# Performance work log

Hardware: AMD Instinct MI355X
Metric: run time of the kernel (lower is better)

## Reference

```python
import jax, jax.numpy as jnp
import numpy as np

ORDER = 3
N_LANES = 5  # lane ids 1..5 (0 = background)
EPS_DEN = 1e-5
RIDGE = 1e-6  # tiny jitter so the 4x4 normal-equation solve is well-posed (matches lstsq on full-rank data)


def setup_inputs() -> dict:
    key = jax.random.key(0)
    k1, k2 = jax.random.split(key)
    hnet_params = jax.random.normal(k1, (8, 6), dtype=jnp.float32)
    instance_label = jax.random.randint(k2, (8, 256, 512), 0, N_LANES + 1).astype(jnp.int64)
    return {"hnet_params": hnet_params, "instance_label": instance_label}


def reference(hnet_params, instance_label):
    B, Hh, Ww = instance_label.shape
    N = Hh * Ww
    p = hnet_params
    z = jnp.zeros((B,), p.dtype)
    o = jnp.ones((B,), p.dtype)
    # H = [[p0,p1,p2],[0,p3,p4],[0,p5,1]]
    Hm = jnp.stack([
        jnp.stack([p[:, 0], p[:, 1], p[:, 2]], -1),
        jnp.stack([z, p[:, 3], p[:, 4]], -1),
        jnp.stack([z, p[:, 5], o], -1),
    ], axis=1)  # [B,3,3]

    yy, xx = jnp.meshgrid(jnp.arange(Hh), jnp.arange(Ww), indexing='ij')
    P = jnp.stack([xx.reshape(-1), yy.reshape(-1), jnp.ones((N,), jnp.int32)]).astype(jnp.float32)  # [3,N]
    Pp = jnp.einsum('bij,jn->bin', Hm, P)  # [B,3,N]
    den = Pp[:, 2]
    den = jnp.where(jnp.abs(den) < EPS_DEN, jnp.full_like(den, EPS_DEN), den)
    xp = Pp[:, 0] / den  # [B,N]
    yp = Pp[:, 1] / den  # [B,N]

    exps = jnp.arange(ORDER, -1, -1)  # powers order..0
    Y = yp[..., None] ** exps  # [B,N,k]

    lane_ids = jnp.arange(1, N_LANES + 1)
    m = (instance_label.reshape(B, 1, N) == lane_ids[None, :, None]).astype(jnp.float32)  # [B,L,N]
    cnt = m.sum(-1)  # [B,L]
    cnt_safe = jnp.maximum(cnt, 1.0)

    # weighted normal equations per (batch, lane): (Y^T M Y) w = Y^T M x'
    A = jnp.einsum('bln,bni,bnj->blij', m, Y, Y)
    rhs = jnp.einsum('bln,bni,bn->bli', m, Y, xp)
    k = ORDER + 1
    A = A + RIDGE * jnp.eye(k, dtype=A.dtype)
    w = jnp.linalg.solve(A, rhs[..., None])[..., 0]  # [B,L,k]

    x_pred = jnp.einsum('bni,bli->bln', Y, w)  # [B,L,N]
    mse = (m * (xp[:, None, :] - x_pred) ** 2).sum(-1) / cnt_safe
    mad = (m * jnp.abs(den)[:, None, :]).sum(-1) / cnt_safe
    lane_loss = mse * mad  # [B,L]

    valid = (cnt >= ORDER + 1).astype(jnp.float32)
    nv = valid.sum()
    loss = jnp.where(nv > 0, (valid * lane_loss).sum() / jnp.maximum(nv, 1.0), 0.0)
    return loss
```

## Files before the change

### kernel.cpp

```cpp
#include <hip/hip_runtime.h>

#define BB 8
#define HH 256
#define WW 512
#define NLANES 5
#define KORD 4
#define RIDGE_D 1e-6
#define EPS_DEN_F 1e-5f

__global__ void row_hist_kernel(const int* __restrict__ labels,
                                int* __restrict__ stats) {
    const int row  = blockIdx.x;
    const int lane = threadIdx.x;
    const int* rp = labels + (size_t)row * WW;

    int c[NLANES], sx[NLANES], sxx[NLANES];
#pragma unroll
    for (int l = 0; l < NLANES; ++l) { c[l] = 0; sx[l] = 0; sxx[l] = 0; }

#pragma unroll
    for (int h = 0; h < 2; ++h) {
        const int j0 = h * 256 + lane * 4;
        const int4 v = *reinterpret_cast<const int4*>(rp + j0);
        const int vv[4] = {v.x, v.y, v.z, v.w};
#pragma unroll
        for (int q = 0; q < 4; ++q) {
            const int j   = j0 + q;
            const int lab = vv[q];
#pragma unroll
            for (int l = 0; l < NLANES; ++l) {
                const int mm = (lab == l + 1) ? 1 : 0;
                c[l]   += mm;
                sx[l]  += mm * j;
                sxx[l] += mm * j * j;
            }
        }
    }

#pragma unroll
    for (int l = 0; l < NLANES; ++l) {
#pragma unroll
        for (int off = 32; off > 0; off >>= 1) {
            c[l]   += __shfl_down(c[l],   off);
            sx[l]  += __shfl_down(sx[l],  off);
            sxx[l] += __shfl_down(sxx[l], off);
        }
    }

    if (lane == 0) {
        const int b = row >> 8;
        const int i = row & 255;
#pragma unroll
        for (int l = 0; l < NLANES; ++l) {
            int* o = stats + (((b * NLANES + l) * HH + i) * 3);
            o[0] = c[l]; o[1] = sx[l]; o[2] = sxx[l];
        }
    }
}

__global__ void lane_fit_kernel(const float* __restrict__ hp,
                                const int* __restrict__ stats,
                                double* __restrict__ out_ll,
                                double* __restrict__ out_valid) {
    const int blk  = blockIdx.x;
    const int b    = blk / NLANES;
    const int l    = blk % NLANES;
    const int lane = threadIdx.x;

    const float p0 = hp[b * 6 + 0];
    const float p1 = hp[b * 6 + 1];
    const float p2 = hp[b * 6 + 2];
    const float p3 = hp[b * 6 + 3];
    const float p5 = hp[b * 6 + 5];
    const float p4 = hp[b * 6 + 4];

    const int* sb = stats + ((b * NLANES + l) * HH) * 3;

    double A[10];
    double r[4];
    double mad = 0.0, cnt = 0.0;
#pragma unroll
    for (int u = 0; u < 10; ++u) A[u] = 0.0;
#pragma unroll
    for (int u = 0; u < 4; ++u)  r[u] = 0.0;

#pragma unroll
    for (int k = 0; k < 4; ++k) {
        const int i = lane + 64 * k;
        const float yf = (float)i;
        float den = p5 * yf + 1.0f;
        if (fabsf(den) < EPS_DEN_F) den = EPS_DEN_F;
        const float ypf = (p3 * yf + p4) / den;
        const float qf  = p1 * yf + p2;

        const double dend = (double)den;
        const double yp   = (double)ypf;
        const double Yv[4] = { yp * yp * yp, yp * yp, yp, 1.0 };

        const int* s = sb + i * 3;
        const double cd  = (double)s[0];
        const double sxd = (double)s[1];
        const double a0  = (double)p0 / dend;
        const double bq  = (double)qf / dend;
        const double rw  = a0 * sxd + bq * cd;

        int idx = 0;
#pragma unroll
        for (int u = 0; u < 4; ++u)
#pragma unroll
            for (int v2 = u; v2 < 4; ++v2)
                A[idx++] += cd * Yv[u] * Yv[v2];
#pragma unroll
        for (int u = 0; u < 4; ++u) r[u] += Yv[u] * rw;

        mad += cd * fabs(dend);
        cnt += cd;
    }

#pragma unroll
    for (int u = 0; u < 10; ++u)
#pragma unroll
        for (int off = 32; off > 0; off >>= 1) A[u] += __shfl_down(A[u], off);
#pragma unroll
    for (int u = 0; u < 4; ++u)
#pragma unroll
        for (int off = 32; off > 0; off >>= 1) r[u] += __shfl_down(r[u], off);
#pragma unroll
    for (int off = 32; off > 0; off >>= 1) { mad += __shfl_down(mad, off);
                                             cnt += __shfl_down(cnt, off); }

    double wl[4] = {0.0, 0.0, 0.0, 0.0};
    if (lane == 0) {
        double M[4][5];
        int idx = 0;
        for (int u = 0; u < 4; ++u)
            for (int v2 = u; v2 < 4; ++v2) {
                M[u][v2] = A[idx];
                M[v2][u] = A[idx];
                ++idx;
            }
        for (int u = 0; u < 4; ++u) M[u][u] += RIDGE_D;
        for (int u = 0; u < 4; ++u) M[u][4] = r[u];

        for (int col = 0; col < 4; ++col) {
            int piv = col;
            double pmax = fabs(M[col][col]);
            for (int rr = col + 1; rr < 4; ++rr) {
                const double av = fabs(M[rr][col]);
                if (av > pmax) { pmax = av; piv = rr; }
            }
            if (piv != col)
                for (int cc = col; cc < 5; ++cc) {
                    const double t = M[col][cc]; M[col][cc] = M[piv][cc]; M[piv][cc] = t;
                }
            const double pv = M[col][col];
            const double inv = (pv != 0.0) ? 1.0 / pv : 0.0;
            for (int rr = col + 1; rr < 4; ++rr) {
                const double f = M[rr][col] * inv;
                for (int cc = col; cc < 5; ++cc) M[rr][cc] -= f * M[col][cc];
            }
        }
        for (int u = 3; u >= 0; --u) {
            double acc = M[u][4];
            for (int cc = u + 1; cc < 4; ++cc) acc -= M[u][cc] * wl[cc];
            const double pv = M[u][u];
            wl[u] = (pv != 0.0) ? acc / pv : 0.0;
        }
    }
    double w0 = __shfl(wl[0], 0);
    double w1 = __shfl(wl[1], 0);
    double w2 = __shfl(wl[2], 0);
    double w3 = __shfl(wl[3], 0);

    double msesum = 0.0;
#pragma unroll
    for (int k = 0; k < 4; ++k) {
        const int i = lane + 64 * k;
        const float yf = (float)i;
        float den = p5 * yf + 1.0f;
        if (fabsf(den) < EPS_DEN_F) den = EPS_DEN_F;
        const float ypf = (p3 * yf + p4) / den;
        const float qf  = p1 * yf + p2;

        const double dend = (double)den;
        const double yp   = (double)ypf;
        const int* s = sb + i * 3;
        const double cd   = (double)s[0];
        const double sxd  = (double)s[1];
        const double sxxd = (double)s[2];
        const double a0   = (double)p0 / dend;
        const double bq   = (double)qf / dend;

        const double t = ((w0 * yp + w1) * yp + w2) * yp + w3;
        const double e = bq - t;
        msesum += a0 * a0 * sxxd + 2.0 * a0 * e * sxd + e * e * cd;
    }
#pragma unroll
    for (int off = 32; off > 0; off >>= 1) msesum += __shfl_down(msesum, off);

    if (lane == 0) {
        const double cnt_safe = fmax(cnt, 1.0);
        const double mse = msesum / cnt_safe;
        const double mdm = mad / cnt_safe;
        out_ll[blk]    = mse * mdm;
        out_valid[blk] = (cnt >= (double)KORD) ? 1.0 : 0.0;
    }
}

__global__ void finalize_kernel(const double* __restrict__ ll,
                                const double* __restrict__ valid,
                                float* __restrict__ out) {
    const int lane = threadIdx.x;
    double num = 0.0, nv = 0.0;
    if (lane < BB * NLANES) {
        const double v = valid[lane];
        num = v * ll[lane];
        nv  = v;
    }
#pragma unroll
    for (int off = 32; off > 0; off >>= 1) {
        num += __shfl_down(num, off);
        nv  += __shfl_down(nv,  off);
    }
    if (lane == 0) {
        const double loss = (nv > 0.0) ? num / fmax(nv, 1.0) : 0.0;
        out[0] = (float)loss;
    }
}

extern "C" void kernel_launch(void* const* d_in, const int* in_sizes, int n_in,
                              void* d_out, int out_size, void* d_ws, size_t ws_size,
                              hipStream_t stream) {
    const float* hp     = (const float*)d_in[0];
    const int*   labels = (const int*)d_in[1];
    float*       out    = (float*)d_out;

    int*    stats = (int*)d_ws;
    double* ll    = (double*)((char*)d_ws + BB * NLANES * HH * 3 * sizeof(int));
    double* valid = ll + BB * NLANES;

    row_hist_kernel<<<BB * HH, 64, 0, stream>>>(labels, stats);
    lane_fit_kernel<<<BB * NLANES, 64, 0, stream>>>(hp, stats, ll, valid);
    finalize_kernel<<<1, 64, 0, stream>>>(ll, valid, out);
}
```

Measured before the change: 16.85 us.

## Fuse finalize into lane-fit via atomics and solve 4x4 system redundantly per lane

Removes the finalize kernel launch. Each lane_fit block now atomically accumulates its weighted loss and valid count and increments a counter, and the last block computes the final loss. The accumulators and counter are reset inside row_hist_kernel. The wave reductions switch to xor shuffles so every lane holds the totals and solves an unrolled, pivot-free symmetric elimination itself, which removes the single-lane solve and the broadcast. Dropping pivoting can change numerics on ill-conditioned systems, and the double atomics make the summation order nondeterministic.

```diff
diff --git a/kernel.cpp b/kernel.cpp
--- a/kernel.cpp
+++ b/kernel.cpp
@@ -8,8 +8,18 @@
 #define RIDGE_D 1e-6
 #define EPS_DEN_F 1e-5f
 
+#define STATS_INTS (BB * NLANES * HH * 3)
+
 __global__ void row_hist_kernel(const int* __restrict__ labels,
-                                int* __restrict__ stats) {
+                                int* __restrict__ stats,
+                                double* __restrict__ acc,
+                                unsigned int* __restrict__ counter) {
+    if (blockIdx.x == 0 && threadIdx.x == 0) {
+        acc[0] = 0.0;
+        acc[1] = 0.0;
+        *counter = 0u;
+    }
+
     const int row  = blockIdx.x;
     const int lane = threadIdx.x;
     const int* rp = labels + (size_t)row * WW;
@@ -60,8 +70,9 @@
 
 __global__ void lane_fit_kernel(const float* __restrict__ hp,
                                 const int* __restrict__ stats,
-                                double* __restrict__ out_ll,
-                                double* __restrict__ out_valid) {
+                                double* __restrict__ acc,
+                                unsigned int* __restrict__ counter,
+                                float* __restrict__ out) {
     const int blk  = blockIdx.x;
     const int b    = blk / NLANES;
     const int l    = blk % NLANES;
@@ -71,8 +82,8 @@
     const float p1 = hp[b * 6 + 1];
     const float p2 = hp[b * 6 + 2];
     const float p3 = hp[b * 6 + 3];
+    const float p4 = hp[b * 6 + 4];
     const float p5 = hp[b * 6 + 5];
-    const float p4 = hp[b * 6 + 4];
 
     const int* sb = stats + ((b * NLANES + l) * HH) * 3;
 
@@ -120,57 +131,46 @@
 #pragma unroll
     for (int u = 0; u < 10; ++u)
 #pragma unroll
-        for (int off = 32; off > 0; off >>= 1) A[u] += __shfl_down(A[u], off);
+        for (int off = 32; off > 0; off >>= 1) A[u] += __shfl_xor(A[u], off);
 #pragma unroll
     for (int u = 0; u < 4; ++u)
 #pragma unroll
-        for (int off = 32; off > 0; off >>= 1) r[u] += __shfl_down(r[u], off);
-#pragma unroll
-    for (int off = 32; off > 0; off >>= 1) { mad += __shfl_down(mad, off);
-                                             cnt += __shfl_down(cnt, off); }
-
-    double wl[4] = {0.0, 0.0, 0.0, 0.0};
-    if (lane == 0) {
-        double M[4][5];
-        int idx = 0;
-        for (int u = 0; u < 4; ++u)
-            for (int v2 = u; v2 < 4; ++v2) {
-                M[u][v2] = A[idx];
-                M[v2][u] = A[idx];
-                ++idx;
-            }
-        for (int u = 0; u < 4; ++u) M[u][u] += RIDGE_D;
-        for (int u = 0; u < 4; ++u) M[u][4] = r[u];
-
-        for (int col = 0; col < 4; ++col) {
-            int piv = col;
-            double pmax = fabs(M[col][col]);
-            for (int rr = col + 1; rr < 4; ++rr) {
-                const double av = fabs(M[rr][col]);
-                if (av > pmax) { pmax = av; piv = rr; }
-            }
-            if (piv != col)
-                for (int cc = col; cc < 5; ++cc) {
-                    const double t = M[col][cc]; M[col][cc] = M[piv][cc]; M[piv][cc] = t;
-                }
-            const double pv = M[col][col];
-            const double inv = (pv != 0.0) ? 1.0 / pv : 0.0;
-            for (int rr = col + 1; rr < 4; ++rr) {
-                const double f = M[rr][col] * inv;
-                for (int cc = col; cc < 5; ++cc) M[rr][cc] -= f * M[col][cc];
-            }
-        }
-        for (int u = 3; u >= 0; --u) {
-            double acc = M[u][4];
-            for (int cc = u + 1; cc < 4; ++cc) acc -= M[u][cc] * wl[cc];
-            const double pv = M[u][u];
-            wl[u] = (pv != 0.0) ? acc / pv : 0.0;
-        }
-    }
-    double w0 = __shfl(wl[0], 0);
-    double w1 = __shfl(wl[1], 0);
-    double w2 = __shfl(wl[2], 0);
-    double w3 = __shfl(wl[3], 0);
+        for (int off = 32; off > 0; off >>= 1) r[u] += __shfl_xor(r[u], off);
+#pragma unroll
+    for (int off = 32; off > 0; off >>= 1) { mad += __shfl_xor(mad, off);
+                                             cnt += __shfl_xor(cnt, off); }
+
+    double m00 = A[0] + RIDGE_D, m01 = A[1],           m02 = A[2],           m03 = A[3];
+    double m11 = A[4] + RIDGE_D, m12 = A[5],           m13 = A[6];
+    double m22 = A[7] + RIDGE_D, m23 = A[8];
+    double m33 = A[9] + RIDGE_D;
+    double r0 = r[0], r1 = r[1], r2 = r[2], r3 = r[3];
+
+    const double inv0 = 1.0 / m00;
+    {
+        const double f10 = m01 * inv0, f20 = m02 * inv0, f30 = m03 * inv0;
+        m11 -= f10 * m01; m12 -= f10 * m02; m13 -= f10 * m03;
+        m22 -= f20 * m02; m23 -= f20 * m03;
+        m33 -= f30 * m03;
+        r1  -= f10 * r0;  r2  -= f20 * r0;  r3  -= f30 * r0;
+    }
+    const double inv1 = 1.0 / m11;
+    {
+        const double f21 = m12 * inv1, f31 = m13 * inv1;
+        m22 -= f21 * m12; m23 -= f21 * m13;
+        m33 -= f31 * m13;
+        r2  -= f21 * r1;  r3  -= f31 * r1;
+    }
+    const double inv2 = 1.0 / m22;
+    {
+        const double f32v = m23 * inv2;
+        m33 -= f32v * m23;
+        r3  -= f32v * r2;
+    }
+    const double w3 = (m33 != 0.0) ? r3 / m33 : 0.0;
+    const double w2 = (r2 - m23 * w3) * inv2;
+    const double w1 = (r1 - m12 * w2 - m13 * w3) * inv1;
+    const double w0 = (r0 - m01 * w1 - m02 * w2 - m03 * w3) * inv0;
 
     double msesum = 0.0;
 #pragma unroll
@@ -202,29 +202,19 @@
         const double cnt_safe = fmax(cnt, 1.0);
         const double mse = msesum / cnt_safe;
         const double mdm = mad / cnt_safe;
-        out_ll[blk]    = mse * mdm;
-        out_valid[blk] = (cnt >= (double)KORD) ? 1.0 : 0.0;
-    }
-}
-
-__global__ void finalize_kernel(const double* __restrict__ ll,
-                                const double* __restrict__ valid,
-                                float* __restrict__ out) {
-    const int lane = threadIdx.x;
-    double num = 0.0, nv = 0.0;
-    if (lane < BB * NLANES) {
-        const double v = valid[lane];
-        num = v * ll[lane];
-        nv  = v;
-    }
-#pragma unroll
-    for (int off = 32; off > 0; off >>= 1) {
-        num += __shfl_down(num, off);
-        nv  += __shfl_down(nv,  off);
-    }
-    if (lane == 0) {
-        const double loss = (nv > 0.0) ? num / fmax(nv, 1.0) : 0.0;
-        out[0] = (float)loss;
+        const double ll  = mse * mdm;
+        const double vv  = (cnt >= (double)KORD) ? 1.0 : 0.0;
+
+        atomicAdd(&acc[0], vv * ll);
+        atomicAdd(&acc[1], vv);
+        __threadfence();
+        const unsigned int prev = atomicAdd(counter, 1u);
+        if (prev == (unsigned int)(BB * NLANES - 1)) {
+            const double num = atomicAdd(&acc[0], 0.0);
+            const double nv  = atomicAdd(&acc[1], 0.0);
+            const double loss = (nv > 0.0) ? num / fmax(nv, 1.0) : 0.0;
+            out[0] = (float)loss;
+        }
     }
 }
 
@@ -235,11 +225,10 @@
     const int*   labels = (const int*)d_in[1];
     float*       out    = (float*)d_out;
 
-    int*    stats = (int*)d_ws;
-    double* ll    = (double*)((char*)d_ws + BB * NLANES * HH * 3 * sizeof(int));
-    double* valid = ll + BB * NLANES;
-
-    row_hist_kernel<<<BB * HH, 64, 0, stream>>>(labels, stats);
-    lane_fit_kernel<<<BB * NLANES, 64, 0, stream>>>(hp, stats, ll, valid);
-    finalize_kernel<<<1, 64, 0, stream>>>(ll, valid, out);
+    int*          stats   = (int*)d_ws;
+    double*       acc     = (double*)((char*)d_ws + STATS_INTS * sizeof(int));
+    unsigned int* counter = (unsigned int*)(acc + 2);
+
+    row_hist_kernel<<<BB * HH, 64, 0, stream>>>(labels, stats, acc, counter);
+    lane_fit_kernel<<<BB * NLANES, 64, 0, stream>>>(hp, stats, acc, counter, out);
 }
```

Result: faster. 15.40 us (-8.6%).
